# Performance work log

Hardware: AMD Instinct MI355X
Metric: run time of the kernel (lower is better)

Reference implementation:

```python
import jax, jax.numpy as jnp
import numpy as np

N, M, C, F = 100000, 12, 64, 41
SH_DIM = 9  # lmax=2 -> 1+3+5
_INV_SQRT_4PI = 0.28209479177387814  # 1/sqrt(4*pi)


def spherical_harmonics_l2(vec):
    """e3nn real SH, lmax=2, normalize=True, normalization='integral'. vec: [..., 3]."""
    r = jnp.sqrt(jnp.sum(vec * vec, axis=-1, keepdims=True) + 1e-12)
    u = vec / r
    x, y, z = u[..., 0], u[..., 1], u[..., 2]
    s3, s15, s5 = jnp.sqrt(3.0), jnp.sqrt(15.0), jnp.sqrt(5.0)
    sh = jnp.stack([
        jnp.ones_like(x),                              # l=0
        s3 * x, s3 * y, s3 * z,                        # l=1 (e3nn order x,y,z)
        s15 * x * z,                                   # l=2
        s15 * x * y,
        s5 * (y * y - 0.5 * (x * x + z * z)),
        s15 * y * z,
        0.5 * s15 * (z * z - x * x),
    ], axis=-1)
    return sh * _INV_SQRT_4PI  # component -> integral normalization


def setup_inputs() -> dict:
    key = jax.random.key(0)
    ks = jax.random.split(key, 9)
    atom_fea = jax.random.normal(ks[0], (N, C), jnp.float32)
    nbr_fea = jax.random.normal(ks[1], (N, M, F), jnp.float32)
    nbr_idx = jax.random.randint(ks[2], (N, M), 0, N)
    pos = jax.random.normal(ks[3], (N, 3), jnp.float32)
    # radial MLP params (Linear(F,F) -> Softplus -> Linear(F, SH_DIM))
    w1 = jax.random.normal(ks[4], (F, F), jnp.float32) / np.sqrt(F)
    b1 = jnp.zeros((F,), jnp.float32)
    w2 = jax.random.normal(ks[5], (F, SH_DIM), jnp.float32) / np.sqrt(F)
    b2 = jnp.zeros((SH_DIM,), jnp.float32)
    # FullyConnectedTensorProduct weights: single path (0e,0e,0e), uvw -> [C_in, C_out]
    tp_w = jax.random.normal(ks[6], (C, C), jnp.float32)
    return {"atom_fea": atom_fea, "nbr_fea": nbr_fea, "nbr_idx": nbr_idx,
            "pos": pos, "w1": w1, "b1": b1, "w2": w2, "b2": b2, "tp_w": tp_w}


def reference(atom_fea, nbr_fea, nbr_idx, pos, w1, b1, w2, b2, tp_w):
    n, m = nbr_idx.shape
    src = nbr_idx.reshape(-1)                       # [N*M]
    h_j = atom_fea[src]                             # gather: [N*M, C]
    # radial MLP
    R = jax.nn.softplus(nbr_fea.reshape(n * m, -1) @ w1 + b1) @ w2 + b2  # [N*M, 9]
    # spherical harmonics of r_ij (dst is row index i, repeated M times)
    vec = pos[src].reshape(n, m, 3) - pos[:, None, :]
    Y = spherical_harmonics_l2(vec).reshape(n * m, SH_DIM)
    W = R * Y                                       # [N*M, 9]
    # FullyConnectedTensorProduct (Cx0e) x (0e+1o+2e) -> Cx0e: only the
    # scalar (l=0) channel of W couples; path normalization 1/sqrt(fan_in=C).
    msg = (h_j * W[:, :1]) @ (tp_w / np.sqrt(h_j.shape[-1]))  # [N*M, C]
    # scatter-mean with dst = arange(N) repeated M times == mean over M axis
    out = msg.reshape(n, m, -1).mean(axis=1)        # [N, C]
    return out
```

## Files before the change

### kernel.cpp

```cpp
#include <hip/hip_runtime.h>

#define N_ROWS 100000
#define M_NBR  12
#define C_DIM  64
#define F_DIM  41
#define E_TOT  (N_ROWS * M_NBR)

typedef _Float16 half8 __attribute__((ext_vector_type(8)));
typedef float float4v __attribute__((ext_vector_type(4)));

#define EPITCH 68

__device__ __forceinline__ void split8(const float (&v)[8], half8& hi, half8& lo) {
    #pragma unroll
    for (int i = 0; i < 8; ++i) {
        const _Float16 h = (_Float16)v[i];
        hi[i] = h;
        lo[i] = (_Float16)(v[i] - (float)h);
    }
}

__global__ __launch_bounds__(256) void edge_mlp_mfma_kernel(
    const float* __restrict__ nbr_fea,
    const float* __restrict__ w1,
    const float* __restrict__ b1,
    const float* __restrict__ w2,
    const float* __restrict__ b2,
    float* __restrict__ s_out)
{
    __shared__ float lx[128 * EPITCH];

    const int tid  = threadIdx.x;
    const int lane = tid & 63;
    const int wv   = tid >> 6;
    const int n15  = lane & 15;
    const int g    = lane >> 4;
    const long base = (long)blockIdx.x * 128;

    {
        const float4* g4 = (const float4*)(nbr_fea + base * F_DIM);
        for (int i = tid; i < 1312; i += 256) {
            const float4 v = g4[i];
            const int f = 4 * i;
            int r = f / F_DIM;
            int c = f - r * F_DIM;
            const float vv[4] = {v.x, v.y, v.z, v.w};
            #pragma unroll
            for (int t = 0; t < 4; ++t) {
                lx[r * EPITCH + c] = vv[t];
                if (++c == F_DIM) { c = 0; ++r; }
            }
        }
        for (int i = tid; i < 128 * 23; i += 256) {
            const int r = i / 23;
            const int c = F_DIM + (i - r * 23);
            lx[r * EPITCH + c] = 0.0f;
        }
    }

    half8 Bh[3][2], Bl[3][2];
    #pragma unroll
    for (int nt = 0; nt < 3; ++nt) {
        const int j = nt * 16 + n15;
        #pragma unroll
        for (int ks = 0; ks < 2; ++ks) {
            float v[8];
            #pragma unroll
            for (int i = 0; i < 8; ++i) {
                const int k = ks * 32 + g * 8 + i;
                v[i] = (j < F_DIM && k < F_DIM) ? w1[k * F_DIM + j] : 0.0f;
            }
            split8(v, Bh[nt][ks], Bl[nt][ks]);
        }
    }

    __syncthreads();

    float4v acc[2][3];
    #pragma unroll
    for (int mt = 0; mt < 2; ++mt)
        #pragma unroll
        for (int nt = 0; nt < 3; ++nt)
            #pragma unroll
            for (int i = 0; i < 4; ++i) acc[mt][nt][i] = 0.0f;

    #pragma unroll
    for (int mt = 0; mt < 2; ++mt) {
        const int row = wv * 32 + mt * 16 + n15;
        #pragma unroll
        for (int ks = 0; ks < 2; ++ks) {
            const float* src = lx + row * EPITCH + ks * 32 + g * 8;
            float av[8];
            *(float4*)(av)     = *(const float4*)(src);
            *(float4*)(av + 4) = *(const float4*)(src + 4);
            half8 ah, al;
            split8(av, ah, al);
            #pragma unroll
            for (int nt = 0; nt < 3; ++nt) {
                acc[mt][nt] = __builtin_amdgcn_mfma_f32_16x16x32_f16(ah, Bh[nt][ks], acc[mt][nt], 0, 0, 0);
                acc[mt][nt] = __builtin_amdgcn_mfma_f32_16x16x32_f16(al, Bh[nt][ks], acc[mt][nt], 0, 0, 0);
                acc[mt][nt] = __builtin_amdgcn_mfma_f32_16x16x32_f16(ah, Bl[nt][ks], acc[mt][nt], 0, 0, 0);
            }
        }
    }

    float b1v[3], w2v[3];
    #pragma unroll
    for (int nt = 0; nt < 3; ++nt) {
        const int j = nt * 16 + n15;
        b1v[nt] = (j < F_DIM) ? b1[j] : 0.0f;
        w2v[nt] = (j < F_DIM) ? w2[j * 9] : 0.0f;
    }
    const float b2v   = b2[0];
    const float scale = 0.28209479177387814f / 12.0f;

    #pragma unroll
    for (int mt = 0; mt < 2; ++mt) {
        float p[4];
        #pragma unroll
        for (int r = 0; r < 4; ++r) {
            float sum = 0.0f;
            #pragma unroll
            for (int nt = 0; nt < 3; ++nt) {
                const float v  = acc[mt][nt][r] + b1v[nt];
                const float sp = fmaxf(v, 0.0f) + __logf(1.0f + __expf(-fabsf(v)));
                sum = fmaf(sp, w2v[nt], sum);
            }
            p[r] = sum;
        }
        #pragma unroll
        for (int m = 1; m < 16; m <<= 1) {
            #pragma unroll
            for (int r = 0; r < 4; ++r) p[r] += __shfl_xor(p[r], m, 64);
        }
        if (n15 == 0) {
            #pragma unroll
            for (int r = 0; r < 4; ++r) {
                const long e = base + wv * 32 + mt * 16 + g * 4 + r;
                s_out[e] = (p[r] + b2v) * scale;
            }
        }
    }
}

__global__ __launch_bounds__(256) void atom_transform_mfma_kernel(
    const float* __restrict__ atom_fea,
    const float* __restrict__ tp_w,
    float* __restrict__ afT)
{
    __shared__ float lx[128 * EPITCH];

    const int tid  = threadIdx.x;
    const int lane = tid & 63;
    const int wv   = tid >> 6;
    const int n15  = lane & 15;
    const int g    = lane >> 4;
    const long row0 = (long)blockIdx.x * 128;
    const int nrow = (N_ROWS - row0) < 128 ? (int)(N_ROWS - row0) : 128;

    {
        const float4* g4 = (const float4*)(atom_fea + row0 * C_DIM);
        for (int i = tid; i < 128 * 16; i += 256) {
            const int r  = i >> 4;
            const int c4 = i & 15;
            const float4 v = (r < nrow) ? g4[r * 16 + c4] : make_float4(0.f, 0.f, 0.f, 0.f);
            *(float4*)(lx + r * EPITCH + c4 * 4) = v;
        }
    }
    __syncthreads();

    float4v acc[2][4];
    #pragma unroll
    for (int mt = 0; mt < 2; ++mt)
        #pragma unroll
        for (int nt = 0; nt < 4; ++nt)
            #pragma unroll
            for (int i = 0; i < 4; ++i) acc[mt][nt][i] = 0.0f;

    #pragma unroll
    for (int ks = 0; ks < 2; ++ks) {
        half8 Th[4], Tl[4];
        #pragma unroll
        for (int nt = 0; nt < 4; ++nt) {
            const int j = nt * 16 + n15;
            float v[8];
            #pragma unroll
            for (int i = 0; i < 8; ++i) {
                const int k = ks * 32 + g * 8 + i;
                v[i] = tp_w[k * C_DIM + j] * 0.125f;
            }
            split8(v, Th[nt], Tl[nt]);
        }
        #pragma unroll
        for (int mt = 0; mt < 2; ++mt) {
            const int row = wv * 32 + mt * 16 + n15;
            const float* src = lx + row * EPITCH + ks * 32 + g * 8;
            float av[8];
            *(float4*)(av)     = *(const float4*)(src);
            *(float4*)(av + 4) = *(const float4*)(src + 4);
            half8 ah, al;
            split8(av, ah, al);
            #pragma unroll
            for (int nt = 0; nt < 4; ++nt) {
                acc[mt][nt] = __builtin_amdgcn_mfma_f32_16x16x32_f16(ah, Th[nt], acc[mt][nt], 0, 0, 0);
                acc[mt][nt] = __builtin_amdgcn_mfma_f32_16x16x32_f16(al, Th[nt], acc[mt][nt], 0, 0, 0);
                acc[mt][nt] = __builtin_amdgcn_mfma_f32_16x16x32_f16(ah, Tl[nt], acc[mt][nt], 0, 0, 0);
            }
        }
    }

    #pragma unroll
    for (int mt = 0; mt < 2; ++mt) {
        #pragma unroll
        for (int r = 0; r < 4; ++r) {
            const long row = row0 + wv * 32 + mt * 16 + g * 4 + r;
            if (row < N_ROWS) {
                #pragma unroll
                for (int nt = 0; nt < 4; ++nt)
                    afT[row * C_DIM + nt * 16 + n15] = acc[mt][nt][r];
            }
        }
    }
}

__global__ __launch_bounds__(256) void gather_kernel(
    const float* __restrict__ afT,
    const int*   __restrict__ nbr_idx,
    const float* __restrict__ s,
    float* __restrict__ out)
{
    const int tid  = threadIdx.x;
    const int lane = tid & 63;
    const int wv   = tid >> 6;
    const int q    = lane >> 4;
    const int c4   = (lane & 15) * 4;

    const int row0 = blockIdx.x * 32 + wv * 8;

    #pragma unroll
    for (int ch = 0; ch < 2; ++ch) {
        int r = row0 + ch * 4 + q;
        const int*   ir = nbr_idx + r * M_NBR;
        const float* sr = s       + r * M_NBR;
        float4 acc = make_float4(0.f, 0.f, 0.f, 0.f);
        #pragma unroll
        for (int j = 0; j < M_NBR; ++j) {
            int   idx = ir[j];
            float sv  = sr[j];
            const float4 a = *(const float4*)(afT + (long)idx * C_DIM + c4);
            acc.x = fmaf(sv, a.x, acc.x);
            acc.y = fmaf(sv, a.y, acc.y);
            acc.z = fmaf(sv, a.z, acc.z);
            acc.w = fmaf(sv, a.w, acc.w);
        }
        *(float4*)(out + (long)r * C_DIM + c4) = acc;
    }
}

__global__ __launch_bounds__(256) void gather_transform_kernel(
    const float* __restrict__ atom_fea,
    const int*   __restrict__ nbr_idx,
    const float* __restrict__ s,
    const float* __restrict__ tp_w,
    float* __restrict__ out)
{
    __shared__ float accL[64 * C_DIM];
    const int tid = threadIdx.x;
    const int c  = tid & 63;
    const int rq = tid >> 6;

    float Tc[64];
    #pragma unroll
    for (int k = 0; k < 64; ++k) Tc[k] = tp_w[k * 64 + c] * 0.125f;

    const int row0 = blockIdx.x * 64;
    for (int i = 0; i < 16; ++i) {
        int r = row0 + rq * 16 + i;
        float a = 0.0f;
        if (r < N_ROWS) {
            const int*   ir = nbr_idx + (long)r * M_NBR;
            const float* sr = s       + (long)r * M_NBR;
            #pragma unroll
            for (int j = 0; j < M_NBR; ++j)
                a = fmaf(sr[j], atom_fea[(long)ir[j] * C_DIM + c], a);
        }
        accL[(rq * 16 + i) * C_DIM + c] = a;
    }
    __syncthreads();
    for (int i = 0; i < 16; ++i) {
        int rl = rq * 16 + i;
        int r  = row0 + rl;
        if (r >= N_ROWS) continue;
        const float* ar = accL + rl * C_DIM;
        float o = 0.0f;
        #pragma unroll
        for (int k = 0; k < 64; ++k) o = fmaf(ar[k], Tc[k], o);
        out[(long)r * C_DIM + c] = o;
    }
}

extern "C" void kernel_launch(void* const* d_in, const int* in_sizes, int n_in,
                              void* d_out, int out_size, void* d_ws, size_t ws_size,
                              hipStream_t stream) {
    const float* atom_fea = (const float*)d_in[0];
    const float* nbr_fea  = (const float*)d_in[1];
    const int*   nbr_idx  = (const int*)  d_in[2];
    const float* w1   = (const float*)d_in[4];
    const float* b1   = (const float*)d_in[5];
    const float* w2   = (const float*)d_in[6];
    const float* b2   = (const float*)d_in[7];
    const float* tp_w = (const float*)d_in[8];

    float* s   = (float*)d_ws;
    float* out = (float*)d_out;

    const int blocksA = E_TOT / 128;
    edge_mlp_mfma_kernel<<<blocksA, 256, 0, stream>>>(nbr_fea, w1, b1, w2, b2, s);

    const size_t sBytes   = (size_t)E_TOT * sizeof(float);
    const size_t afTBytes = (size_t)N_ROWS * C_DIM * sizeof(float);

    if (ws_size >= sBytes + afTBytes) {
        float* afT = (float*)((char*)d_ws + sBytes);
        const int blocksT = (N_ROWS + 127) / 128;
        atom_transform_mfma_kernel<<<blocksT, 256, 0, stream>>>(atom_fea, tp_w, afT);
        const int blocksG = N_ROWS / 32;
        gather_kernel<<<blocksG, 256, 0, stream>>>(afT, nbr_idx, s, out);
    } else {
        const int blocksB = (N_ROWS + 63) / 64;
        gather_transform_kernel<<<blocksB, 256, 0, stream>>>(atom_fea, nbr_idx, s, tp_w, out);
    }
}
```

Before: 389.3 us.

## Use single-pass fp16 MFMA for edge MLP and fp16 transformed atom features

Drops the hi/lo fp16 split in the edge MLP, so each tile uses one MFMA instead of three. The bias is folded into the GEMM through a constant-one column, and the weights are pre-packed into fp16 by a small prep kernel. The transformed atom features are stored as fp16, which halves the bytes read by the random-access neighbour gather. This trades accuracy for less compute and memory traffic, and adds one tiny kernel launch.

New measurement: 354.4 us. 9.0% less time.

```diff
diff --git a/kernel.cpp b/kernel.cpp
--- a/kernel.cpp
+++ b/kernel.cpp
@@ -7,9 +7,11 @@
 #define E_TOT  (N_ROWS * M_NBR)
 
 typedef _Float16 half8 __attribute__((ext_vector_type(8)));
+typedef _Float16 half4v __attribute__((ext_vector_type(4)));
 typedef float float4v __attribute__((ext_vector_type(4)));
 
-#define EPITCH 68
+#define EPITCH   68
+#define EPITCH_H 72
 
 __device__ __forceinline__ void split8(const float (&v)[8], half8& hi, half8& lo) {
     #pragma unroll
@@ -20,15 +22,42 @@
     }
 }
 
+__global__ __launch_bounds__(64) void prep_edge_B(
+    const float* __restrict__ w1,
+    const float* __restrict__ b1,
+    _Float16* __restrict__ bpack)
+{
+    const int lane = threadIdx.x;
+    const int n15 = lane & 15, g = lane >> 4;
+    #pragma unroll
+    for (int nt = 0; nt < 3; ++nt) {
+        const int j = nt * 16 + n15;
+        #pragma unroll
+        for (int ks = 0; ks < 2; ++ks) {
+            half8 v;
+            #pragma unroll
+            for (int i = 0; i < 8; ++i) {
+                const int k = ks * 32 + g * 8 + i;
+                float f = 0.0f;
+                if (j < F_DIM) {
+                    if (k < F_DIM)       f = w1[k * F_DIM + j];
+                    else if (k == F_DIM) f = b1[j];
+                }
+                v[i] = (_Float16)f;
+            }
+            *(half8*)(bpack + ((nt * 2 + ks) * 64 + lane) * 8) = v;
+        }
+    }
+}
+
 __global__ __launch_bounds__(256) void edge_mlp_mfma_kernel(
     const float* __restrict__ nbr_fea,
-    const float* __restrict__ w1,
-    const float* __restrict__ b1,
+    const _Float16* __restrict__ bpack,
     const float* __restrict__ w2,
     const float* __restrict__ b2,
     float* __restrict__ s_out)
 {
-    __shared__ float lx[128 * EPITCH];
+    __shared__ _Float16 lx[128 * EPITCH_H];
 
     const int tid  = threadIdx.x;
     const int lane = tid & 63;
@@ -47,68 +76,50 @@
             const float vv[4] = {v.x, v.y, v.z, v.w};
             #pragma unroll
             for (int t = 0; t < 4; ++t) {
-                lx[r * EPITCH + c] = vv[t];
+                lx[r * EPITCH_H + c] = (_Float16)vv[t];
                 if (++c == F_DIM) { c = 0; ++r; }
             }
         }
         for (int i = tid; i < 128 * 23; i += 256) {
             const int r = i / 23;
             const int c = F_DIM + (i - r * 23);
-            lx[r * EPITCH + c] = 0.0f;
-        }
-    }
-
-    half8 Bh[3][2], Bl[3][2];
+            lx[r * EPITCH_H + c] = (c == F_DIM) ? (_Float16)1.0f : (_Float16)0.0f;
+        }
+    }
+
+    half8 Bh[3][2];
+    #pragma unroll
+    for (int nt = 0; nt < 3; ++nt)
+        #pragma unroll
+        for (int ks = 0; ks < 2; ++ks)
+            Bh[nt][ks] = *(const half8*)(bpack + ((nt * 2 + ks) * 64 + lane) * 8);
+
+    __syncthreads();
+
+    float4v acc[2][3];
+    #pragma unroll
+    for (int mt = 0; mt < 2; ++mt)
+        #pragma unroll
+        for (int nt = 0; nt < 3; ++nt)
+            #pragma unroll
+            for (int i = 0; i < 4; ++i) acc[mt][nt][i] = 0.0f;
+
+    #pragma unroll
+    for (int mt = 0; mt < 2; ++mt) {
+        const int row = wv * 32 + mt * 16 + n15;
+        #pragma unroll
+        for (int ks = 0; ks < 2; ++ks) {
+            const half8 a = *(const half8*)(lx + row * EPITCH_H + ks * 32 + g * 8);
+            #pragma unroll
+            for (int nt = 0; nt < 3; ++nt)
+                acc[mt][nt] = __builtin_amdgcn_mfma_f32_16x16x32_f16(a, Bh[nt][ks], acc[mt][nt], 0, 0, 0);
+        }
+    }
+
+    float w2v[3];
     #pragma unroll
     for (int nt = 0; nt < 3; ++nt) {
         const int j = nt * 16 + n15;
-        #pragma unroll
-        for (int ks = 0; ks < 2; ++ks) {
-            float v[8];
-            #pragma unroll
-            for (int i = 0; i < 8; ++i) {
-                const int k = ks * 32 + g * 8 + i;
-                v[i] = (j < F_DIM && k < F_DIM) ? w1[k * F_DIM + j] : 0.0f;
-            }
-            split8(v, Bh[nt][ks], Bl[nt][ks]);
-        }
-    }
-
-    __syncthreads();
-
-    float4v acc[2][3];
-    #pragma unroll
-    for (int mt = 0; mt < 2; ++mt)
-        #pragma unroll
-        for (int nt = 0; nt < 3; ++nt)
-            #pragma unroll
-            for (int i = 0; i < 4; ++i) acc[mt][nt][i] = 0.0f;
-
-    #pragma unroll
-    for (int mt = 0; mt < 2; ++mt) {
-        const int row = wv * 32 + mt * 16 + n15;
-        #pragma unroll
-        for (int ks = 0; ks < 2; ++ks) {
-            const float* src = lx + row * EPITCH + ks * 32 + g * 8;
-            float av[8];
-            *(float4*)(av)     = *(const float4*)(src);
-            *(float4*)(av + 4) = *(const float4*)(src + 4);
-            half8 ah, al;
-            split8(av, ah, al);
-            #pragma unroll
-            for (int nt = 0; nt < 3; ++nt) {
-                acc[mt][nt] = __builtin_amdgcn_mfma_f32_16x16x32_f16(ah, Bh[nt][ks], acc[mt][nt], 0, 0, 0);
-                acc[mt][nt] = __builtin_amdgcn_mfma_f32_16x16x32_f16(al, Bh[nt][ks], acc[mt][nt], 0, 0, 0);
-                acc[mt][nt] = __builtin_amdgcn_mfma_f32_16x16x32_f16(ah, Bl[nt][ks], acc[mt][nt], 0, 0, 0);
-            }
-        }
-    }
-
-    float b1v[3], w2v[3];
-    #pragma unroll
-    for (int nt = 0; nt < 3; ++nt) {
-        const int j = nt * 16 + n15;
-        b1v[nt] = (j < F_DIM) ? b1[j] : 0.0f;
         w2v[nt] = (j < F_DIM) ? w2[j * 9] : 0.0f;
     }
     const float b2v   = b2[0];
@@ -122,7 +133,7 @@
             float sum = 0.0f;
             #pragma unroll
             for (int nt = 0; nt < 3; ++nt) {
-                const float v  = acc[mt][nt][r] + b1v[nt];
+                const float v  = acc[mt][nt][r];
                 const float sp = fmaxf(v, 0.0f) + __logf(1.0f + __expf(-fabsf(v)));
                 sum = fmaf(sp, w2v[nt], sum);
             }
@@ -146,7 +157,7 @@
 __global__ __launch_bounds__(256) void atom_transform_mfma_kernel(
     const float* __restrict__ atom_fea,
     const float* __restrict__ tp_w,
-    float* __restrict__ afT)
+    _Float16* __restrict__ afT)
 {
     __shared__ float lx[128 * EPITCH];
 
@@ -217,14 +228,14 @@
             if (row < N_ROWS) {
                 #pragma unroll
                 for (int nt = 0; nt < 4; ++nt)
-                    afT[row * C_DIM + nt * 16 + n15] = acc[mt][nt][r];
+                    afT[row * C_DIM + nt * 16 + n15] = (_Float16)acc[mt][nt][r];
             }
         }
     }
 }
 
 __global__ __launch_bounds__(256) void gather_kernel(
-    const float* __restrict__ afT,
+    const _Float16* __restrict__ afT,
     const int*   __restrict__ nbr_idx,
     const float* __restrict__ s,
     float* __restrict__ out)
@@ -247,11 +258,11 @@
         for (int j = 0; j < M_NBR; ++j) {
             int   idx = ir[j];
             float sv  = sr[j];
-            const float4 a = *(const float4*)(afT + (long)idx * C_DIM + c4);
-            acc.x = fmaf(sv, a.x, acc.x);
-            acc.y = fmaf(sv, a.y, acc.y);
-            acc.z = fmaf(sv, a.z, acc.z);
-            acc.w = fmaf(sv, a.w, acc.w);
+            const half4v a = *(const half4v*)(afT + (long)idx * C_DIM + c4);
+            acc.x = fmaf(sv, (float)a[0], acc.x);
+            acc.y = fmaf(sv, (float)a[1], acc.y);
+            acc.z = fmaf(sv, (float)a[2], acc.z);
+            acc.w = fmaf(sv, (float)a[3], acc.w);
         }
         *(float4*)(out + (long)r * C_DIM + c4) = acc;
     }
@@ -311,17 +322,20 @@
     const float* b2   = (const float*)d_in[7];
     const float* tp_w = (const float*)d_in[8];
 
-    float* s   = (float*)d_ws;
-    float* out = (float*)d_out;
+    _Float16* bpack = (_Float16*)d_ws;
+    float*    s     = (float*)((char*)d_ws + 8192);
+    float*    out   = (float*)d_out;
+
+    const size_t sBytes    = (size_t)E_TOT * sizeof(float);
+    const size_t afTBytes  = (size_t)N_ROWS * C_DIM * sizeof(_Float16);
+
+    prep_edge_B<<<1, 64, 0, stream>>>(w1, b1, bpack);
 
     const int blocksA = E_TOT / 128;
-    edge_mlp_mfma_kernel<<<blocksA, 256, 0, stream>>>(nbr_fea, w1, b1, w2, b2, s);
-
-    const size_t sBytes   = (size_t)E_TOT * sizeof(float);
-    const size_t afTBytes = (size_t)N_ROWS * C_DIM * sizeof(float);
-
-    if (ws_size >= sBytes + afTBytes) {
-        float* afT = (float*)((char*)d_ws + sBytes);
+    edge_mlp_mfma_kernel<<<blocksA, 256, 0, stream>>>(nbr_fea, bpack, w2, b2, s);
+
+    if (ws_size >= 8192 + sBytes + afTBytes) {
+        _Float16* afT = (_Float16*)((char*)d_ws + 8192 + sBytes);
         const int blocksT = (N_ROWS + 127) / 128;
         atom_transform_mfma_kernel<<<blocksT, 256, 0, stream>>>(atom_fea, tp_w, afT);
         const int blocksG = N_ROWS / 32;
```
